# Kernel tuning notes

Measured on AMD Instinct MI355X. Metric: run time of the kernel, lower is better.

The kernel has to match this reference:

```python
import jax, jax.numpy as jnp
import numpy as np

B, T, C = 4, 2048, 2048
N_HEAD = 16
HEAD_DIM = C // N_HEAD  # 128
ROPE_BASE = 10000.0


def rope_cache(dim, seq_len, base=ROPE_BASE):
    inv_freq = 1.0 / (base ** (jnp.arange(0, dim, 2, dtype=jnp.float32) / dim))
    t = jnp.arange(seq_len, dtype=jnp.float32)
    freqs = jnp.outer(t, inv_freq)  # [T, dim//2]
    return jnp.cos(freqs), jnp.sin(freqs)


def apply_rope(q, k, cos, sin):
    # q, k: [B, H, T, D], interleaved-pair rotation
    q1, q2 = q[..., 0::2], q[..., 1::2]
    k1, k2 = k[..., 0::2], k[..., 1::2]
    c = cos[None, None, :, :]
    s = sin[None, None, :, :]
    q_rot = jnp.stack([q1 * c - q2 * s, q1 * s + q2 * c], axis=-1).reshape(q.shape)
    k_rot = jnp.stack([k1 * c - k2 * s, k1 * s + k2 * c], axis=-1).reshape(k.shape)
    return q_rot, k_rot


def setup_inputs() -> dict:
    key = jax.random.key(0)
    k1, k2, k3 = jax.random.split(key, 3)
    x = jax.random.normal(k1, (B, T, C), dtype=jnp.float32)
    W_attn = jax.random.normal(k2, (3 * C, C), dtype=jnp.float32) * (1.0 / np.sqrt(C))
    W_proj = jax.random.normal(k3, (C, C), dtype=jnp.float32) * (1.0 / np.sqrt(C))
    return {"x": x, "W_attn": W_attn, "W_proj": W_proj}


def reference(x, W_attn, W_proj):
    Bx, Tx, Cx = x.shape
    qkv = jnp.einsum('btc,fc->btf', x, W_attn)  # [B, T, 3C]
    q, k, v = jnp.split(qkv, 3, axis=-1)
    # [B, H, T, D]
    q = q.reshape(Bx, Tx, N_HEAD, HEAD_DIM).transpose(0, 2, 1, 3)
    k = k.reshape(Bx, Tx, N_HEAD, HEAD_DIM).transpose(0, 2, 1, 3)
    v = v.reshape(Bx, Tx, N_HEAD, HEAD_DIM).transpose(0, 2, 1, 3)
    cos, sin = rope_cache(HEAD_DIM, Tx)
    q, k = apply_rope(q, k, cos, sin)
    scale = 1.0 / np.sqrt(HEAD_DIM)
    scores = jnp.einsum('bhqd,bhkd->bhqk', q, k) * scale
    causal = jnp.tril(jnp.ones((Tx, Tx), dtype=bool))
    scores = jnp.where(causal[None, None, :, :], scores, jnp.finfo(scores.dtype).min)
    attn = jax.nn.softmax(scores, axis=-1)
    y = jnp.einsum('bhqk,bhkd->bhqd', attn, v)
    y = y.transpose(0, 2, 1, 3).reshape(Bx, Tx, Cx)
    return jnp.einsum('btc,fc->btf', y, W_proj)
```

## Files before the change

### kernel.cpp

```cpp
#include <hip/hip_runtime.h>
#include <stdint.h>

#define TT 2048
#define CC 2048
#define NHEAD 16
#define HD 128
#define NB 4
#define MTOT (NB*TT)
#define KD 2048
#define NT 32

typedef __attribute__((ext_vector_type(8))) short bf16x8;
typedef __attribute__((ext_vector_type(4))) float f32x4;
typedef __attribute__((ext_vector_type(16))) float f32x16;
typedef __attribute__((ext_vector_type(4))) unsigned u32x4;

__device__ __forceinline__ unsigned short f2bf(float f) {
  unsigned u = __float_as_uint(f);
  u += 0x7FFF + ((u >> 16) & 1);
  return (unsigned short)(u >> 16);
}
__device__ __forceinline__ float bf2f(unsigned short h) {
  return __uint_as_float(((unsigned)h) << 16);
}

__device__ __forceinline__ void gl_lds16(const unsigned short* g, short* l) {
  __builtin_amdgcn_global_load_lds(
      (const __attribute__((address_space(1))) void*)(g),
      (__attribute__((address_space(3))) void*)(l), 16, 0, 0);
}

#define MFMA16(a, b, c) __builtin_amdgcn_mfma_f32_16x16x32_bf16((a), (b), (c), 0, 0, 0)
#define MFMA32(a, b, c) __builtin_amdgcn_mfma_f32_32x32x16_bf16((a), (b), (c), 0, 0, 0)

#define PRE_MFMA() do { \
  __builtin_amdgcn_s_barrier(); \
  asm volatile("s_waitcnt lgkmcnt(0)" ::: "memory"); \
  __builtin_amdgcn_s_setprio(1); \
} while(0)
#define POST_MFMA() do { \
  __builtin_amdgcn_s_setprio(0); \
  __builtin_amdgcn_s_barrier(); \
  __builtin_amdgcn_sched_barrier(0); \
} while(0)

__global__ void k_f2b(const float* __restrict__ in, unsigned short* __restrict__ out, int n4) {
  int i = blockIdx.x * 256 + threadIdx.x;
  if (i >= n4) return;
  float4 v = reinterpret_cast<const float4*>(in)[i];
  ushort4 o;
  o.x = f2bf(v.x); o.y = f2bf(v.y); o.z = f2bf(v.z); o.w = f2bf(v.w);
  reinterpret_cast<ushort4*>(out)[i] = o;
}

__global__ void k_rope_tab(float* __restrict__ tab) {
  int t = blockIdx.x, i = threadIdx.x;
  double inv = exp2(-(double)i * (13.287712379549449062 / 64.0));
  double ang = (double)t * inv;
  tab[(t*64 + i)*2 + 0] = (float)cos(ang);
  tab[(t*64 + i)*2 + 1] = (float)sin(ang);
}

__device__ __forceinline__ void gemm256_core(
    const unsigned short* __restrict__ Ag,
    const unsigned short* __restrict__ Bg,
    int m0, int n0, short* lds, f32x4 (&acc)[8][4])
{
  const int tid = threadIdx.x;
  const int wid = tid >> 6, lane = tid & 63;
  const int wm = wid >> 2, wn = wid & 3;
  const int r15 = lane & 15, hi4 = lane >> 4;
  const int srow = wid*8 + (lane >> 3);
  const int schunk = (lane & 7) ^ (lane >> 3);

  const f32x4 fz = {0.f, 0.f, 0.f, 0.f};
#pragma unroll
  for (int i = 0; i < 8; i++)
#pragma unroll
    for (int j = 0; j < 4; j++) acc[i][j] = fz;

  int aoff0[8];
#pragma unroll
  for (int mi = 0; mi < 8; mi++) {
    int row = wm*128 + mi*16 + r15;
    aoff0[mi] = row*64 + ((hi4 ^ (row & 7))*8);
  }
  int boff0[4];
#pragma unroll
  for (int ni = 0; ni < 4; ni++) {
    int row = wn*64 + ni*16 + r15;
    boff0[ni] = row*64 + ((hi4 ^ (row & 7))*8);
  }

#define STAGE(G, L, GROW0, KT) do { \
    gl_lds16((G) + (size_t)((GROW0) + srow)*KD + (KT) + schunk*8, (L) + wid*512); \
    gl_lds16((G) + (size_t)((GROW0) + 64 + srow)*KD + (KT) + schunk*8, (L) + 4096 + wid*512); \
  } while(0)

  STAGE(Ag, lds,                        m0,       0);
  STAGE(Ag, lds + 8192,                 m0 + 128, 0);
  STAGE(Bg, lds + 32768,                n0,       0);
  STAGE(Bg, lds + 32768 + 8192,         n0 + 128, 0);
  STAGE(Bg, lds + 32768 + 16384,        n0,       64);
  STAGE(Bg, lds + 32768 + 16384 + 8192, n0 + 128, 64);
  asm volatile("s_waitcnt vmcnt(4)" ::: "memory");
  __builtin_amdgcn_s_barrier();
  __builtin_amdgcn_sched_barrier(0);

#pragma unroll 1
  for (int t = 0; t < NT; t++) {
    const int db = t & 1;
    short* Ab = lds + db*16384;
    short* Bb = lds + 32768 + db*16384;
    short* An = lds + (db ^ 1)*16384;
    const int kt = t*64;
    const bool stA = (t < NT - 1);
    const bool stB = (t < NT - 2);

    bf16x8 a[8], b[4][2];
#pragma unroll
    for (int mi = 0; mi < 8; mi++)
      a[mi] = *reinterpret_cast<const bf16x8*>(Ab + aoff0[mi]);
#pragma unroll
    for (int ni = 0; ni < 4; ni++) {
      b[ni][0] = *reinterpret_cast<const bf16x8*>(Bb + boff0[ni]);
      b[ni][1] = *reinterpret_cast<const bf16x8*>(Bb + (boff0[ni] ^ 32));
    }
    if (stA) {
      STAGE(Ag, An,        m0,       kt + 64);
      STAGE(Ag, An + 8192, m0 + 128, kt + 64);
    }
    PRE_MFMA();
#pragma unroll
    for (int mi = 0; mi < 8; mi++)
#pragma unroll
      for (int ni = 0; ni < 4; ni++)
        acc[mi][ni] = MFMA16(a[mi], b[ni][0], acc[mi][ni]);
    POST_MFMA();

#pragma unroll
    for (int mi = 0; mi < 8; mi++)
      a[mi] = *reinterpret_cast<const bf16x8*>(Ab + (aoff0[mi] ^ 32));
    if (stB) {
      STAGE(Bg, Bb,        n0,       kt + 128);
      STAGE(Bg, Bb + 8192, n0 + 128, kt + 128);
    }
    if (t >= NT - 2) asm volatile("s_waitcnt vmcnt(0)" ::: "memory");
    else             asm volatile("s_waitcnt vmcnt(4)" ::: "memory");
    PRE_MFMA();
#pragma unroll
    for (int mi = 0; mi < 8; mi++)
#pragma unroll
      for (int ni = 0; ni < 4; ni++)
        acc[mi][ni] = MFMA16(a[mi], b[ni][1], acc[mi][ni]);
    POST_MFMA();
  }
#undef STAGE
}

__global__ __launch_bounds__(512, 2) void k_qkv(
    const unsigned short* __restrict__ xb,
    const unsigned short* __restrict__ wab,
    const float* __restrict__ tab,
    unsigned short* __restrict__ qr,
    unsigned short* __restrict__ kr,
    unsigned short* __restrict__ vt)
{
  __shared__ __align__(16) short lds[65536];
  f32x4 acc[8][4];
  int bid = blockIdx.x;
  int swz = (bid & 7)*96 + (bid >> 3);
  int m0 = (swz / 24)*256, n0 = (swz % 24)*256;
  gemm256_core(xb, wab, m0, n0, lds, acc);

  int tid = threadIdx.x, wid = tid >> 6, lane = tid & 63;
  int wm = wid >> 2, wn = wid & 3, r15 = lane & 15, hi4 = lane >> 4;
  int nw0 = n0 + wn*64;
  int which = nw0 >> 11;
  int h = (nw0 & 2047) >> 7;
#pragma unroll
  for (int mi = 0; mi < 8; mi++) {
    int m_base = m0 + wm*128 + mi*16 + hi4*4;
    int b = m_base >> 11;
    int t0 = m_base & (TT - 1);
#pragma unroll
    for (int ni = 0; ni < 4; ni++) {
      int d = (nw0 & 127) + ni*16 + r15;
      if (which == 2) {
        ushort4 pv;
        pv.x = f2bf(acc[mi][ni][0]); pv.y = f2bf(acc[mi][ni][1]);
        pv.z = f2bf(acc[mi][ni][2]); pv.w = f2bf(acc[mi][ni][3]);
        *reinterpret_cast<ushort4*>(vt + ((size_t)((b*NHEAD + h)*HD + d))*TT + t0) = pv;
      } else {
        unsigned short* dst = (which == 0) ? qr : kr;
        size_t base = ((size_t)(b*NHEAD + h)*TT + t0)*HD + d;
        int j = d >> 1;
        bool odd = (d & 1);
#pragma unroll
        for (int r = 0; r < 4; r++) {
          float v = acc[mi][ni][r];
          float pv = __shfl_xor(v, 1);
          float2 cs = *reinterpret_cast<const float2*>(tab + ((size_t)(t0 + r)*64 + j)*2);
          float res = odd ? (pv*cs.y + v*cs.x) : (v*cs.x - pv*cs.y);
          dst[base + (size_t)r*HD] = f2bf(res);
        }
      }
    }
  }
}

__global__ __launch_bounds__(512, 2) void k_proj(
    const unsigned short* __restrict__ yb,
    const unsigned short* __restrict__ wpb,
    float* __restrict__ out)
{
  __shared__ __align__(16) short lds[65536];
  f32x4 acc[8][4];
  int bid = blockIdx.x;
  int swz = (bid & 7)*32 + (bid >> 3);
  int m0 = (swz / 8)*256, n0 = (swz % 8)*256;
  gemm256_core(yb, wpb, m0, n0, lds, acc);

  int tid = threadIdx.x, wid = tid >> 6, lane = tid & 63;
  int wm = wid >> 2, wn = wid & 3, r15 = lane & 15, hi4 = lane >> 4;
  int nw0 = n0 + wn*64;
#pragma unroll
  for (int mi = 0; mi < 8; mi++) {
    int m = m0 + wm*128 + mi*16 + hi4*4;
#pragma unroll
    for (int ni = 0; ni < 4; ni++) {
      int n = nw0 + ni*16 + r15;
#pragma unroll
      for (int r = 0; r < 4; r++)
        out[(size_t)(m + r)*CC + n] = acc[mi][ni][r];
    }
  }
}

__global__ __launch_bounds__(512, 1) void k_attn(
    const unsigned short* __restrict__ qr,
    const unsigned short* __restrict__ kr,
    const unsigned short* __restrict__ vt,
    unsigned short* __restrict__ yb)
{
  __shared__ __align__(16) short Ks[2][64*128];
  __shared__ __align__(16) short Vs[2][128*64];
  __shared__ float alds[8][32];
  int bid = blockIdx.x;
  int bh = bid & 63, pr = bid >> 6;
  int tid = threadIdx.x, w = tid >> 6, lane = tid & 63;
  int l31 = lane & 31, hi = lane >> 5;
  const unsigned short* qg = qr + (size_t)bh*TT*HD;
  const unsigned short* kg = kr + (size_t)bh*TT*HD;
  const unsigned short* vg = vt + (size_t)bh*HD*TT;
  const float scale = 0.08838834764831845f;
  int b = bh >> 4, h = bh & 15;

  int ksoff[2], vsoff[2];
#pragma unroll
  for (int i = 0; i < 2; i++) {
    int c = w*2 + i;
    int rK = c*4 + (lane >> 4);
    int cK = (lane & 15) ^ (rK & 7);
    ksoff[i] = rK*HD + cK*8;
    int dV = c*8 + (lane >> 3);
    int cV = (lane & 7) ^ (dV & 7);
    vsoff[i] = dV*TT + cV*8;
  }

#define STAGE_KV(BUF, KV0) do { \
    _Pragma("unroll") \
    for (int i_ = 0; i_ < 2; i_++) { \
      gl_lds16(kg + (size_t)(KV0)*HD + ksoff[i_], &Ks[BUF][(w*2 + i_)*512]); \
      gl_lds16(vg + (KV0) + vsoff[i_],            &Vs[BUF][(w*2 + i_)*512]); \
    } \
  } while(0)

#pragma unroll 1
  for (int ph = 0; ph < 2; ph++) {
    int qb = ph ? (7 - pr) : pr;
    int qlo = qb*256 + w*32;
    int qgi = qlo + l31;
    bf16x8 qf[8];
#pragma unroll
    for (int kk = 0; kk < 8; kk++)
      qf[kk] = *reinterpret_cast<const bf16x8*>(qg + (size_t)qgi*HD + kk*16 + hi*8);

    f32x16 ao[4];
#pragma unroll
    for (int dt = 0; dt < 4; dt++)
#pragma unroll
      for (int r = 0; r < 16; r++) ao[dt][r] = 0.f;
    float mrow = -3.0e38f, lsum = 0.f;
    int ntiles = 4*qb + 4;

    STAGE_KV(0, 0);
    __syncthreads();
    int cur = 0;

#pragma unroll 1
    for (int it = 0; it < ntiles; ++it) {
      int kv0 = it*64;
      if (it + 1 < ntiles) STAGE_KV(cur ^ 1, kv0 + 64);
      if (kv0 <= qlo + 31) {
        const short* Kc = Ks[cur];
        const short* Vc = Vs[cur];
        bool full = (kv0 + 63 <= qlo);
        f32x16 s0, s1;
#pragma unroll
        for (int r = 0; r < 16; r++) { s0[r] = 0.f; s1[r] = 0.f; }
        __builtin_amdgcn_s_setprio(1);
#pragma unroll
        for (int kk = 0; kk < 8; kk++) {
          int row0 = l31, row1 = 32 + l31;
          int ch0 = ((2*kk + hi) ^ (row0 & 7));
          int ch1 = ((2*kk + hi) ^ (row1 & 7));
          bf16x8 kf0 = *reinterpret_cast<const bf16x8*>((const char*)Kc + row0*256 + ch0*16);
          bf16x8 kf1 = *reinterpret_cast<const bf16x8*>((const char*)Kc + row1*256 + ch1*16);
          s0 = MFMA32(kf0, qf[kk], s0);
          s1 = MFMA32(kf1, qf[kk], s1);
        }
        __builtin_amdgcn_s_setprio(0);
        float p[32];
#pragma unroll
        for (int r = 0; r < 16; r++) {
          int kvl = (r & 3) + 8*(r >> 2) + 4*hi;
          float v0 = s0[r]*scale, v1 = s1[r]*scale;
          if (!full) {
            v0 = (kv0 + kvl      <= qgi) ? v0 : -3.0e38f;
            v1 = (kv0 + 32 + kvl <= qgi) ? v1 : -3.0e38f;
          }
          p[r] = v0; p[16 + r] = v1;
        }
        float t16[16];
#pragma unroll
        for (int i = 0; i < 16; i++) t16[i] = fmaxf(p[i], p[i + 16]);
#pragma unroll
        for (int i = 0; i < 8; i++) t16[i] = fmaxf(t16[i], t16[i + 8]);
#pragma unroll
        for (int i = 0; i < 4; i++) t16[i] = fmaxf(t16[i], t16[i + 4]);
        float mx = fmaxf(fmaxf(t16[0], t16[1]), fmaxf(t16[2], t16[3]));
        mx = fmaxf(mx, __shfl_xor(mx, 32));
        bool defer = __all(mx <= mrow + 8.f);
        if (!defer) {
          float mnew = fmaxf(mrow, mx);
          float alpha = __expf(mrow - mnew);
          mrow = mnew;
          lsum *= alpha;
          if (lane < 32) alds[w][lane] = alpha;
#pragma unroll
          for (int r = 0; r < 16; r++) {
            int ql = (r & 3) + 8*(r >> 2) + 4*hi;
            float av = alds[w][ql];
#pragma unroll
            for (int dt = 0; dt < 4; dt++) ao[dt][r] *= av;
          }
        }
#pragma unroll
        for (int i = 0; i < 32; i++) p[i] = __expf(p[i] - mrow);
#pragma unroll
        for (int i = 0; i < 16; i++) t16[i] = p[i] + p[i + 16];
#pragma unroll
        for (int i = 0; i < 8; i++) t16[i] = t16[i] + t16[i + 8];
#pragma unroll
        for (int i = 0; i < 4; i++) t16[i] = t16[i] + t16[i + 4];
        float rs = (t16[0] + t16[1]) + (t16[2] + t16[3]);
        rs += __shfl_xor(rs, 32);
        lsum += rs;
        bf16x8 pa[4];
#pragma unroll
        for (int ks = 0; ks < 4; ks++) {
          const int base = (ks >> 1)*16 + (ks & 1)*8;
          unsigned a0, a1, b0, b1;
          asm("v_cvt_pk_bf16_f32 %0, %1, %2" : "=v"(a0) : "v"(p[base + 0]), "v"(p[base + 1]));
          asm("v_cvt_pk_bf16_f32 %0, %1, %2" : "=v"(a1) : "v"(p[base + 2]), "v"(p[base + 3]));
          asm("v_cvt_pk_bf16_f32 %0, %1, %2" : "=v"(b0) : "v"(p[base + 4]), "v"(p[base + 5]));
          asm("v_cvt_pk_bf16_f32 %0, %1, %2" : "=v"(b1) : "v"(p[base + 6]), "v"(p[base + 7]));
          unsigned sa0 = (unsigned)__shfl_xor((int)a0, 32);
          unsigned sa1 = (unsigned)__shfl_xor((int)a1, 32);
          unsigned sb0 = (unsigned)__shfl_xor((int)b0, 32);
          unsigned sb1 = (unsigned)__shfl_xor((int)b1, 32);
          u32x4 pw;
          pw.x = hi ? sb0 : a0;
          pw.y = hi ? sb1 : a1;
          pw.z = hi ? b0 : sa0;
          pw.w = hi ? b1 : sa1;
          pa[ks] = __builtin_bit_cast(bf16x8, pw);
        }
        __builtin_amdgcn_s_setprio(1);
#pragma unroll
        for (int dt = 0; dt < 4; dt++) {
          int d = dt*32 + l31;
#pragma unroll
          for (int ks = 0; ks < 4; ks++) {
            int ch = ((2*ks + hi) ^ (d & 7));
            bf16x8 vf = *reinterpret_cast<const bf16x8*>((const char*)Vc + d*128 + ch*16);
            ao[dt] = MFMA32(pa[ks], vf, ao[dt]);
          }
        }
        __builtin_amdgcn_s_setprio(0);
      }
      __syncthreads();
      cur ^= 1;
    }
    if (lane < 32) alds[w][lane] = 1.0f / lsum;
#pragma unroll
    for (int r = 0; r < 16; r++) {
      int ql = (r & 3) + 8*(r >> 2) + 4*hi;
      float lv = alds[w][ql];
      int t = qlo + ql;
      size_t base = ((size_t)b*TT + t)*CC + h*HD + l31;
#pragma unroll
      for (int dt = 0; dt < 4; dt++)
        yb[base + dt*32] = f2bf(ao[dt][r] * lv);
    }
    __syncthreads();
  }
#undef STAGE_KV
}

extern "C" void kernel_launch(void* const* d_in, const int* in_sizes, int n_in,
                              void* d_out, int out_size, void* d_ws, size_t ws_size,
                              hipStream_t stream) {
  const float* x  = (const float*)d_in[0];
  const float* wa = (const float*)d_in[1];
  const float* wp = (const float*)d_in[2];
  float* out = (float*)d_out;
  char* ws = (char*)d_ws;
  size_t off = 0;
  unsigned short* xb  = (unsigned short*)(ws + off); off += (size_t)MTOT*CC*2;
  unsigned short* wab = (unsigned short*)(ws + off); off += (size_t)3*CC*CC*2;
  unsigned short* wpb = (unsigned short*)(ws + off); off += (size_t)CC*CC*2;
  unsigned short* qr  = (unsigned short*)(ws + off); off += (size_t)MTOT*CC*2;
  unsigned short* kr  = (unsigned short*)(ws + off); off += (size_t)MTOT*CC*2;
  unsigned short* vt  = (unsigned short*)(ws + off); off += (size_t)MTOT*CC*2;
  unsigned short* yb  = (unsigned short*)(ws + off); off += (size_t)MTOT*CC*2;
  float* tab          = (float*)(ws + off);          off += (size_t)TT*64*2*4;

  k_f2b<<<dim3(16384), dim3(256), 0, stream>>>(x,  xb,  MTOT*CC/4);
  k_f2b<<<dim3(12288), dim3(256), 0, stream>>>(wa, wab, 3*CC*CC/4);
  k_f2b<<<dim3(4096),  dim3(256), 0, stream>>>(wp, wpb, CC*CC/4);
  k_rope_tab<<<dim3(TT), dim3(64), 0, stream>>>(tab);
  k_qkv<<<dim3(768), dim3(512), 0, stream>>>(xb, wab, tab, qr, kr, vt);
  k_attn<<<dim3(256), dim3(512), 0, stream>>>(qr, kr, vt, yb);
  k_proj<<<dim3(256), dim3(512), 0, stream>>>(yb, wpb, out);
}
```

Baseline: 411.0 us.

## Restructure GEMM core into quadrant-based ping-pong schedule with finer-grained LDS staging

Reorganizes the 256x256 bf16 GEMM core so each wave computes four 64x32 sub-quadrants, cycling through separate LDS buffers for A/B halves across two k-steps per iteration. Global-to-LDS loads of each half-tile are issued right after that buffer is consumed, which spreads memory traffic between MFMA groups and reuses A fragments across two B halves. Epilogues for the QKV (with RoPE) and projection kernels are remapped to the new accumulator layout. The more intricate vmcnt accounting and buffer reuse ordering risk subtle races, and the per-wave output footprint is now non-contiguous.

Result: no change. 407.5 us (-0.8%).

```diff
diff --git a/kernel.cpp b/kernel.cpp
--- a/kernel.cpp
+++ b/kernel.cpp
@@ -64,7 +64,7 @@
 __device__ __forceinline__ void gemm256_core(
     const unsigned short* __restrict__ Ag,
     const unsigned short* __restrict__ Bg,
-    int m0, int n0, short* lds, f32x4 (&acc)[8][4])
+    int m0, int n0, short* lds, f32x4 (&acc)[2][2][4][2])
 {
   const int tid = threadIdx.x;
   const int wid = tid >> 6, lane = tid & 63;
@@ -75,84 +75,189 @@
 
   const f32x4 fz = {0.f, 0.f, 0.f, 0.f};
 #pragma unroll
-  for (int i = 0; i < 8; i++)
-#pragma unroll
-    for (int j = 0; j < 4; j++) acc[i][j] = fz;
-
-  int aoff0[8];
-#pragma unroll
-  for (int mi = 0; mi < 8; mi++) {
-    int row = wm*128 + mi*16 + r15;
-    aoff0[mi] = row*64 + ((hi4 ^ (row & 7))*8);
-  }
-  int boff0[4];
-#pragma unroll
-  for (int ni = 0; ni < 4; ni++) {
-    int row = wn*64 + ni*16 + r15;
-    boff0[ni] = row*64 + ((hi4 ^ (row & 7))*8);
-  }
+  for (int p = 0; p < 2; p++)
+#pragma unroll
+    for (int q = 0; q < 2; q++)
+#pragma unroll
+      for (int i = 0; i < 4; i++)
+#pragma unroll
+        for (int j = 0; j < 2; j++) acc[p][q][i][j] = fz;
+
+  int aoff[4][2];
+#pragma unroll
+  for (int mi = 0; mi < 4; mi++)
+#pragma unroll
+    for (int kk = 0; kk < 2; kk++) {
+      int row = wm*64 + mi*16 + r15;
+      aoff[mi][kk] = row*64 + (((kk*4 + hi4) ^ (row & 7))*8);
+    }
+  int boff[2][2];
+#pragma unroll
+  for (int ni = 0; ni < 2; ni++)
+#pragma unroll
+    for (int kk = 0; kk < 2; kk++) {
+      int row = wn*32 + ni*16 + r15;
+      boff[ni][kk] = row*64 + (((kk*4 + hi4) ^ (row & 7))*8);
+    }
+
+  short* A0  = lds;            short* A1  = lds + 8192;
+  short* A0b = lds + 16384;    short* A1b = lds + 24576;
+  short* B0l = lds + 32768;    short* B1l = lds + 40960;
+  short* B0b = lds + 49152;    short* B1b = lds + 57344;
 
 #define STAGE(G, L, GROW0, KT) do { \
     gl_lds16((G) + (size_t)((GROW0) + srow)*KD + (KT) + schunk*8, (L) + wid*512); \
     gl_lds16((G) + (size_t)((GROW0) + 64 + srow)*KD + (KT) + schunk*8, (L) + 4096 + wid*512); \
   } while(0)
 
-  STAGE(Ag, lds,                        m0,       0);
-  STAGE(Ag, lds + 8192,                 m0 + 128, 0);
-  STAGE(Bg, lds + 32768,                n0,       0);
-  STAGE(Bg, lds + 32768 + 8192,         n0 + 128, 0);
-  STAGE(Bg, lds + 32768 + 16384,        n0,       64);
-  STAGE(Bg, lds + 32768 + 16384 + 8192, n0 + 128, 64);
-  asm volatile("s_waitcnt vmcnt(4)" ::: "memory");
+  STAGE(Ag, A0,  m0,       0);
+  STAGE(Bg, B0l, n0,       0);
+  STAGE(Bg, B1l, n0 + 128, 0);
+  STAGE(Ag, A1,  m0 + 128, 0);
+  STAGE(Ag, A0b, m0,       64);
+  STAGE(Bg, B0b, n0,       64);
+  STAGE(Bg, B1b, n0 + 128, 64);
+  asm volatile("s_waitcnt vmcnt(0)" ::: "memory");
   __builtin_amdgcn_s_barrier();
   __builtin_amdgcn_sched_barrier(0);
 
+  bf16x8 a[4][2], b0[2][2], b1[2][2];
+
 #pragma unroll 1
-  for (int t = 0; t < NT; t++) {
-    const int db = t & 1;
-    short* Ab = lds + db*16384;
-    short* Bb = lds + 32768 + db*16384;
-    short* An = lds + (db ^ 1)*16384;
-    const int kt = t*64;
-    const bool stA = (t < NT - 1);
-    const bool stB = (t < NT - 2);
-
-    bf16x8 a[8], b[4][2];
-#pragma unroll
-    for (int mi = 0; mi < 8; mi++)
-      a[mi] = *reinterpret_cast<const bf16x8*>(Ab + aoff0[mi]);
-#pragma unroll
-    for (int ni = 0; ni < 4; ni++) {
-      b[ni][0] = *reinterpret_cast<const bf16x8*>(Bb + boff0[ni]);
-      b[ni][1] = *reinterpret_cast<const bf16x8*>(Bb + (boff0[ni] ^ 32));
-    }
-    if (stA) {
-      STAGE(Ag, An,        m0,       kt + 64);
-      STAGE(Ag, An + 8192, m0 + 128, kt + 64);
-    }
-    PRE_MFMA();
-#pragma unroll
-    for (int mi = 0; mi < 8; mi++)
-#pragma unroll
-      for (int ni = 0; ni < 4; ni++)
-        acc[mi][ni] = MFMA16(a[mi], b[ni][0], acc[mi][ni]);
-    POST_MFMA();
-
-#pragma unroll
-    for (int mi = 0; mi < 8; mi++)
-      a[mi] = *reinterpret_cast<const bf16x8*>(Ab + (aoff0[mi] ^ 32));
-    if (stB) {
-      STAGE(Bg, Bb,        n0,       kt + 128);
-      STAGE(Bg, Bb + 8192, n0 + 128, kt + 128);
-    }
-    if (t >= NT - 2) asm volatile("s_waitcnt vmcnt(0)" ::: "memory");
-    else             asm volatile("s_waitcnt vmcnt(4)" ::: "memory");
-    PRE_MFMA();
-#pragma unroll
-    for (int mi = 0; mi < 8; mi++)
-#pragma unroll
-      for (int ni = 0; ni < 4; ni++)
-        acc[mi][ni] = MFMA16(a[mi], b[ni][1], acc[mi][ni]);
+  for (int it = 0; it < 16; it++) {
+    const int kt = it*128;
+    const bool stP = (it < 15);
+
+#pragma unroll
+    for (int mi = 0; mi < 4; mi++) {
+      a[mi][0] = *reinterpret_cast<const bf16x8*>(A0 + aoff[mi][0]);
+      a[mi][1] = *reinterpret_cast<const bf16x8*>(A0 + aoff[mi][1]);
+    }
+#pragma unroll
+    for (int ni = 0; ni < 2; ni++) {
+      b0[ni][0] = *reinterpret_cast<const bf16x8*>(B0l + boff[ni][0]);
+      b0[ni][1] = *reinterpret_cast<const bf16x8*>(B0l + boff[ni][1]);
+    }
+    STAGE(Ag, A1b, m0 + 128, kt + 64);
+    PRE_MFMA();
+#pragma unroll
+    for (int mi = 0; mi < 4; mi++)
+#pragma unroll
+      for (int ni = 0; ni < 2; ni++) {
+        acc[0][0][mi][ni] = MFMA16(a[mi][0], b0[ni][0], acc[0][0][mi][ni]);
+        acc[0][0][mi][ni] = MFMA16(a[mi][1], b0[ni][1], acc[0][0][mi][ni]);
+      }
+    POST_MFMA();
+
+#pragma unroll
+    for (int ni = 0; ni < 2; ni++) {
+      b1[ni][0] = *reinterpret_cast<const bf16x8*>(B1l + boff[ni][0]);
+      b1[ni][1] = *reinterpret_cast<const bf16x8*>(B1l + boff[ni][1]);
+    }
+    if (stP) STAGE(Ag, A0, m0, kt + 128);
+    PRE_MFMA();
+#pragma unroll
+    for (int mi = 0; mi < 4; mi++)
+#pragma unroll
+      for (int ni = 0; ni < 2; ni++) {
+        acc[0][1][mi][ni] = MFMA16(a[mi][0], b1[ni][0], acc[0][1][mi][ni]);
+        acc[0][1][mi][ni] = MFMA16(a[mi][1], b1[ni][1], acc[0][1][mi][ni]);
+      }
+    POST_MFMA();
+
+#pragma unroll
+    for (int mi = 0; mi < 4; mi++) {
+      a[mi][0] = *reinterpret_cast<const bf16x8*>(A1 + aoff[mi][0]);
+      a[mi][1] = *reinterpret_cast<const bf16x8*>(A1 + aoff[mi][1]);
+    }
+    if (stP) STAGE(Bg, B0l, n0, kt + 128);
+    PRE_MFMA();
+#pragma unroll
+    for (int mi = 0; mi < 4; mi++)
+#pragma unroll
+      for (int ni = 0; ni < 2; ni++) {
+        acc[1][1][mi][ni] = MFMA16(a[mi][0], b1[ni][0], acc[1][1][mi][ni]);
+        acc[1][1][mi][ni] = MFMA16(a[mi][1], b1[ni][1], acc[1][1][mi][ni]);
+      }
+    POST_MFMA();
+
+    if (stP) STAGE(Bg, B1l, n0 + 128, kt + 128);
+    if (stP) asm volatile("s_waitcnt vmcnt(6)" ::: "memory");
+    else     asm volatile("s_waitcnt vmcnt(0)" ::: "memory");
+    PRE_MFMA();
+#pragma unroll
+    for (int mi = 0; mi < 4; mi++)
+#pragma unroll
+      for (int ni = 0; ni < 2; ni++) {
+        acc[1][0][mi][ni] = MFMA16(a[mi][0], b0[ni][0], acc[1][0][mi][ni]);
+        acc[1][0][mi][ni] = MFMA16(a[mi][1], b0[ni][1], acc[1][0][mi][ni]);
+      }
+    POST_MFMA();
+
+#pragma unroll
+    for (int mi = 0; mi < 4; mi++) {
+      a[mi][0] = *reinterpret_cast<const bf16x8*>(A0b + aoff[mi][0]);
+      a[mi][1] = *reinterpret_cast<const bf16x8*>(A0b + aoff[mi][1]);
+    }
+#pragma unroll
+    for (int ni = 0; ni < 2; ni++) {
+      b0[ni][0] = *reinterpret_cast<const bf16x8*>(B0b + boff[ni][0]);
+      b0[ni][1] = *reinterpret_cast<const bf16x8*>(B0b + boff[ni][1]);
+    }
+    if (stP) STAGE(Ag, A1, m0 + 128, kt + 128);
+    PRE_MFMA();
+#pragma unroll
+    for (int mi = 0; mi < 4; mi++)
+#pragma unroll
+      for (int ni = 0; ni < 2; ni++) {
+        acc[0][0][mi][ni] = MFMA16(a[mi][0], b0[ni][0], acc[0][0][mi][ni]);
+        acc[0][0][mi][ni] = MFMA16(a[mi][1], b0[ni][1], acc[0][0][mi][ni]);
+      }
+    POST_MFMA();
+
+#pragma unroll
+    for (int ni = 0; ni < 2; ni++) {
+      b1[ni][0] = *reinterpret_cast<const bf16x8*>(B1b + boff[ni][0]);
+      b1[ni][1] = *reinterpret_cast<const bf16x8*>(B1b + boff[ni][1]);
+    }
+    if (stP) STAGE(Ag, A0b, m0, kt + 192);
+    PRE_MFMA();
+#pragma unroll
+    for (int mi = 0; mi < 4; mi++)
+#pragma unroll
+      for (int ni = 0; ni < 2; ni++) {
+        acc[0][1][mi][ni] = MFMA16(a[mi][0], b1[ni][0], acc[0][1][mi][ni]);
+        acc[0][1][mi][ni] = MFMA16(a[mi][1], b1[ni][1], acc[0][1][mi][ni]);
+      }
+    POST_MFMA();
+
+#pragma unroll
+    for (int mi = 0; mi < 4; mi++) {
+      a[mi][0] = *reinterpret_cast<const bf16x8*>(A1b + aoff[mi][0]);
+      a[mi][1] = *reinterpret_cast<const bf16x8*>(A1b + aoff[mi][1]);
+    }
+    if (stP) STAGE(Bg, B0b, n0, kt + 192);
+    PRE_MFMA();
+#pragma unroll
+    for (int mi = 0; mi < 4; mi++)
+#pragma unroll
+      for (int ni = 0; ni < 2; ni++) {
+        acc[1][1][mi][ni] = MFMA16(a[mi][0], b1[ni][0], acc[1][1][mi][ni]);
+        acc[1][1][mi][ni] = MFMA16(a[mi][1], b1[ni][1], acc[1][1][mi][ni]);
+      }
+    POST_MFMA();
+
+    if (stP) STAGE(Bg, B1b, n0 + 128, kt + 192);
+    if (stP) asm volatile("s_waitcnt vmcnt(6)" ::: "memory");
+    else     asm volatile("s_waitcnt vmcnt(0)" ::: "memory");
+    PRE_MFMA();
+#pragma unroll
+    for (int mi = 0; mi < 4; mi++)
+#pragma unroll
+      for (int ni = 0; ni < 2; ni++) {
+        acc[1][0][mi][ni] = MFMA16(a[mi][0], b0[ni][0], acc[1][0][mi][ni]);
+        acc[1][0][mi][ni] = MFMA16(a[mi][1], b0[ni][1], acc[1][0][mi][ni]);
+      }
     POST_MFMA();
   }
 #undef STAGE
@@ -167,7 +272,7 @@
     unsigned short* __restrict__ vt)
 {
   __shared__ __align__(16) short lds[65536];
-  f32x4 acc[8][4];
+  f32x4 acc[2][2][4][2];
   int bid = blockIdx.x;
   int swz = (bid & 7)*96 + (bid >> 3);
   int m0 = (swz / 24)*256, n0 = (swz % 24)*256;
@@ -175,34 +280,39 @@
 
   int tid = threadIdx.x, wid = tid >> 6, lane = tid & 63;
   int wm = wid >> 2, wn = wid & 3, r15 = lane & 15, hi4 = lane >> 4;
-  int nw0 = n0 + wn*64;
-  int which = nw0 >> 11;
-  int h = (nw0 & 2047) >> 7;
-#pragma unroll
-  for (int mi = 0; mi < 8; mi++) {
-    int m_base = m0 + wm*128 + mi*16 + hi4*4;
-    int b = m_base >> 11;
-    int t0 = m_base & (TT - 1);
-#pragma unroll
-    for (int ni = 0; ni < 4; ni++) {
-      int d = (nw0 & 127) + ni*16 + r15;
-      if (which == 2) {
-        ushort4 pv;
-        pv.x = f2bf(acc[mi][ni][0]); pv.y = f2bf(acc[mi][ni][1]);
-        pv.z = f2bf(acc[mi][ni][2]); pv.w = f2bf(acc[mi][ni][3]);
-        *reinterpret_cast<ushort4*>(vt + ((size_t)((b*NHEAD + h)*HD + d))*TT + t0) = pv;
-      } else {
-        unsigned short* dst = (which == 0) ? qr : kr;
-        size_t base = ((size_t)(b*NHEAD + h)*TT + t0)*HD + d;
-        int j = d >> 1;
-        bool odd = (d & 1);
-#pragma unroll
-        for (int r = 0; r < 4; r++) {
-          float v = acc[mi][ni][r];
-          float pv = __shfl_xor(v, 1);
-          float2 cs = *reinterpret_cast<const float2*>(tab + ((size_t)(t0 + r)*64 + j)*2);
-          float res = odd ? (pv*cs.y + v*cs.x) : (v*cs.x - pv*cs.y);
-          dst[base + (size_t)r*HD] = f2bf(res);
+  int which = n0 >> 11;
+#pragma unroll
+  for (int GM = 0; GM < 2; GM++) {
+#pragma unroll
+    for (int mi = 0; mi < 4; mi++) {
+      int m_base = m0 + GM*128 + wm*64 + mi*16 + hi4*4;
+      int b = m_base >> 11;
+      int t0 = m_base & (TT - 1);
+#pragma unroll
+      for (int GN = 0; GN < 2; GN++) {
+        int h = ((n0 & 2047) >> 7) + GN;
+#pragma unroll
+        for (int ni = 0; ni < 2; ni++) {
+          int d = wn*32 + ni*16 + r15;
+          if (which == 2) {
+            ushort4 pv;
+            pv.x = f2bf(acc[GM][GN][mi][ni][0]); pv.y = f2bf(acc[GM][GN][mi][ni][1]);
+            pv.z = f2bf(acc[GM][GN][mi][ni][2]); pv.w = f2bf(acc[GM][GN][mi][ni][3]);
+            *reinterpret_cast<ushort4*>(vt + ((size_t)((b*NHEAD + h)*HD + d))*TT + t0) = pv;
+          } else {
+            unsigned short* dst = (which == 0) ? qr : kr;
+            size_t base = ((size_t)(b*NHEAD + h)*TT + t0)*HD + d;
+            int j = d >> 1;
+            bool odd = (d & 1);
+#pragma unroll
+            for (int r = 0; r < 4; r++) {
+              float v = acc[GM][GN][mi][ni][r];
+              float pv = __shfl_xor(v, 1);
+              float2 cs = *reinterpret_cast<const float2*>(tab + ((size_t)(t0 + r)*64 + j)*2);
+              float res = odd ? (pv*cs.y + v*cs.x) : (v*cs.x - pv*cs.y);
+              dst[base + (size_t)r*HD] = f2bf(res);
+            }
+          }
         }
       }
     }
@@ -215,7 +325,7 @@
     float* __restrict__ out)
 {
   __shared__ __align__(16) short lds[65536];
-  f32x4 acc[8][4];
+  f32x4 acc[2][2][4][2];
   int bid = blockIdx.x;
   int swz = (bid & 7)*32 + (bid >> 3);
   int m0 = (swz / 8)*256, n0 = (swz % 8)*256;
@@ -223,16 +333,21 @@
 
   int tid = threadIdx.x, wid = tid >> 6, lane = tid & 63;
   int wm = wid >> 2, wn = wid & 3, r15 = lane & 15, hi4 = lane >> 4;
-  int nw0 = n0 + wn*64;
-#pragma unroll
-  for (int mi = 0; mi < 8; mi++) {
-    int m = m0 + wm*128 + mi*16 + hi4*4;
-#pragma unroll
-    for (int ni = 0; ni < 4; ni++) {
-      int n = nw0 + ni*16 + r15;
-#pragma unroll
-      for (int r = 0; r < 4; r++)
-        out[(size_t)(m + r)*CC + n] = acc[mi][ni][r];
+#pragma unroll
+  for (int GM = 0; GM < 2; GM++) {
+#pragma unroll
+    for (int mi = 0; mi < 4; mi++) {
+      int m = m0 + GM*128 + wm*64 + mi*16 + hi4*4;
+#pragma unroll
+      for (int GN = 0; GN < 2; GN++) {
+#pragma unroll
+        for (int ni = 0; ni < 2; ni++) {
+          int n = n0 + GN*128 + wn*32 + ni*16 + r15;
+#pragma unroll
+          for (int r = 0; r < 4; r++)
+            out[(size_t)(m + r)*CC + n] = acc[GM][GN][mi][ni][r];
+        }
+      }
     }
   }
 }
```
